# Kernel tuning notes

Measured on AMD Instinct MI355X. Metric: run time of the kernel, lower is better.

## Reference

```python
import jax, jax.numpy as jnp
import numpy as np

SINKHORN_ALPHA = 20.0
WEIGHT_LOSS_ECR = 100.0
OT_MAX_ITER = 100
STOP_THR = 0.005
EPS = 1e-16


def setup_inputs() -> dict:
    key = jax.random.key(0)
    # cost matrix: [num_topics, vocab]
    M = jax.random.uniform(key, (512, 65536), dtype=jnp.float32)
    return {"M": M}


def reference(M) -> jnp.ndarray:
    n, m = M.shape
    a = jnp.full((n, 1), 1.0 / n, dtype=M.dtype)   # row marginal
    b = jnp.full((m, 1), 1.0 / m, dtype=M.dtype)   # col marginal
    u0 = jnp.full((n, 1), 1.0 / n, dtype=M.dtype)
    K = jnp.exp(-M * SINKHORN_ALPHA)               # [n, m]

    def cond_fn(carry):
        u, v, err, cpt = carry
        return (err > STOP_THR) & (cpt < OT_MAX_ITER)

    def body_fn(carry):
        u, v, err, cpt = carry
        v = b / (K.T @ u + EPS)                    # [m, 1]
        u = a / (K @ v + EPS)                      # [n, 1]
        cpt = cpt + 1
        # convergence check every 50 iters (cpt % 50 == 1), matching torch loop
        err = jax.lax.cond(
            cpt % 50 == 1,
            lambda: jnp.sum(jnp.abs(v * (K.T @ u) - b)).astype(err.dtype),
            lambda: err,
        )
        return (u, v, err, cpt)

    init = (u0, jnp.zeros((m, 1), dtype=M.dtype), jnp.asarray(1.0, M.dtype), jnp.asarray(0, jnp.int32))
    u, v, _, _ = jax.lax.while_loop(cond_fn, body_fn, init)

    transp = u * (K * v.T)                         # [n, m] transport plan
    loss_ECR = jnp.sum(transp * M) * WEIGHT_LOSS_ECR
    return loss_ECR
```

## Files before the change

### kernel.cpp

```cpp
#include <hip/hip_runtime.h>

#define NROW 512
#define NCOL 65536
#define BANDS 4

static __device__ __forceinline__ float wave_sum(float x) {
  #pragma unroll
  for (int off = 32; off; off >>= 1) x += __shfl_down(x, off, 64);
  return x;
}

static __device__ __forceinline__ void gbar(int* cnt, int* phase) {
  __syncthreads();
  if (threadIdx.x == 0) {
    int ph = atomicAdd(phase, 0);
    __threadfence();
    if (atomicAdd(cnt, 1) == (int)gridDim.x - 1) {
      atomicExch(cnt, 0);
      __threadfence();
      atomicAdd(phase, 1);
    } else {
      while (atomicAdd(phase, 0) == ph) { __builtin_amdgcn_s_sleep(8); }
    }
    __threadfence();
  }
  __syncthreads();
}

static __device__ __forceinline__ unsigned short f2bf(float f) {
  unsigned int u = __float_as_uint(f);
  u += 0x7FFFu + ((u >> 16) & 1u);
  return (unsigned short)(u >> 16);
}
static __device__ __forceinline__ float bf2f_lo(unsigned int w) {
  return __uint_as_float(w << 16);
}
static __device__ __forceinline__ float bf2f_hi(unsigned int w) {
  return __uint_as_float(w & 0xFFFF0000u);
}

__global__ __launch_bounds__(512)
void k1a_colsum(const float* __restrict__ M, unsigned short* __restrict__ E16,
                float* __restrict__ tPart, float* __restrict__ eA,
                int* __restrict__ bar) {
  const int tid = threadIdx.x, bid = blockIdx.x;
  const int colblk = bid & 255, band = bid >> 8;
  const int chunk = tid & 63;
  const int part  = tid >> 6;
  const int col0  = (colblk << 8) + (chunk << 2);
  const int r0    = (band << 7) + (part << 4);

  __shared__ float sCol[8 * 256];

  if (bid == 0 && tid < 8) eA[tid] = 0.f;
  if (bid == 0 && tid < 2) bar[tid] = 0;

  const float* Mp = M + (size_t)r0 * NCOL + col0;
  unsigned short* Ep = E16 + (size_t)r0 * NCOL + col0;
  float4 cs = {0.f, 0.f, 0.f, 0.f};
  #pragma unroll 8
  for (int rr = 0; rr < 16; ++rr) {
    float4 m = *(const float4*)(Mp + (size_t)rr * NCOL);
    float e0 = __expf(-20.f * m.x), e1 = __expf(-20.f * m.y);
    float e2 = __expf(-20.f * m.z), e3 = __expf(-20.f * m.w);
    cs.x += e0; cs.y += e1; cs.z += e2; cs.w += e3;
    uint2 w;
    w.x = (unsigned int)f2bf(e0) | ((unsigned int)f2bf(e1) << 16);
    w.y = (unsigned int)f2bf(e2) | ((unsigned int)f2bf(e3) << 16);
    *(uint2*)(Ep + (size_t)rr * NCOL) = w;
  }
  *(float4*)(sCol + part * 256 + (chunk << 2)) = cs;
  __syncthreads();
  if (tid < 256) {
    float t = 0.f;
    #pragma unroll
    for (int p = 0; p < 8; ++p) t += sCol[p * 256 + tid];
    tPart[(size_t)band * NCOL + (colblk << 8) + tid] = t;
  }
}

__global__ __launch_bounds__(256)
void k1b_v1(const float* __restrict__ tPart, float* __restrict__ v) {
  const int gid = blockIdx.x * 256 + threadIdx.x;
  const int col0 = gid << 2;
  const float am = 1.0f / NROW, bm = 1.0f / NCOL, EPSV = 1e-16f;
  float4 t = {0.f, 0.f, 0.f, 0.f};
  #pragma unroll
  for (int b = 0; b < BANDS; ++b) {
    float4 p = *(const float4*)(tPart + (size_t)b * NCOL + col0);
    t.x += p.x; t.y += p.y; t.z += p.z; t.w += p.w;
  }
  float4 vv = {bm / (t.x * am + EPSV), bm / (t.y * am + EPSV),
               bm / (t.z * am + EPSV), bm / (t.w * am + EPSV)};
  *(float4*)(v + col0) = vv;
}

__global__ __launch_bounds__(1024)
void k2_rowdot(const unsigned short* __restrict__ E16,
               const float* __restrict__ v, float* __restrict__ u) {
  const int tid = threadIdx.x, row = blockIdx.x;
  const float am = 1.0f / NROW, EPSV = 1e-16f;
  const uint4* E4 = (const uint4*)(E16 + (size_t)row * NCOL);
  const float4* V4 = (const float4*)v;
  __shared__ float sRed[16];

  float acc = 0.f;
  #pragma unroll 4
  for (int it = 0; it < NCOL / 8 / 1024; ++it) {
    const int c = (it << 10) + tid;
    uint4 w = E4[c];
    float4 va = V4[2 * c], vb = V4[2 * c + 1];
    acc += bf2f_lo(w.x) * va.x + bf2f_hi(w.x) * va.y
         + bf2f_lo(w.y) * va.z + bf2f_hi(w.y) * va.w
         + bf2f_lo(w.z) * vb.x + bf2f_hi(w.z) * vb.y
         + bf2f_lo(w.w) * vb.z + bf2f_hi(w.w) * vb.w;
  }
  acc = wave_sum(acc);
  if ((tid & 63) == 0) sRed[tid >> 6] = acc;
  __syncthreads();
  if (tid == 0) {
    float s = 0.f;
    #pragma unroll
    for (int w = 0; w < 16; ++w) s += sRed[w];
    u[row] = am / (s + EPSV);
  }
}

__global__ __launch_bounds__(512)
void k3a_colsum_u(const unsigned short* __restrict__ E16,
                  const float* __restrict__ v, const float* __restrict__ u,
                  float* __restrict__ tPart, float* __restrict__ eA) {
  const int tid = threadIdx.x, bid = blockIdx.x;
  const int colblk = bid & 255, band = bid >> 8;
  const int chunk = tid & 63;
  const int part  = tid >> 6;
  const int col0  = (colblk << 8) + (chunk << 2);
  const int r0l   = part << 4;

  __shared__ float sU[128];
  __shared__ float sCol[8 * 256];
  __shared__ float sRed[8];

  if (tid < 128) sU[tid] = u[(band << 7) + tid];
  __syncthreads();

  const float4 vv = *(const float4*)(v + col0);
  const unsigned short* Ep = E16 + (size_t)((band << 7) + r0l) * NCOL + col0;
  float4 cs = {0.f, 0.f, 0.f, 0.f};
  float lacc = 0.f;
  #pragma unroll 8
  for (int rr = 0; rr < 16; ++rr) {
    uint2 w = *(const uint2*)(Ep + (size_t)rr * NCOL);
    float e0 = bf2f_lo(w.x), e1 = bf2f_hi(w.x);
    float e2 = bf2f_lo(w.y), e3 = bf2f_hi(w.y);
    float us = sU[r0l + rr];
    cs.x = fmaf(e0, us, cs.x);
    cs.y = fmaf(e1, us, cs.y);
    cs.z = fmaf(e2, us, cs.z);
    cs.w = fmaf(e3, us, cs.w);
    float m0 = __logf(e0) * (-0.05f);
    float m1 = __logf(e1) * (-0.05f);
    float m2 = __logf(e2) * (-0.05f);
    float m3 = __logf(e3) * (-0.05f);
    lacc += us * (e0 * m0 * vv.x + e1 * m1 * vv.y
                + e2 * m2 * vv.z + e3 * m3 * vv.w);
  }
  *(float4*)(sCol + part * 256 + (chunk << 2)) = cs;
  lacc = wave_sum(lacc);
  if ((tid & 63) == 0) sRed[tid >> 6] = lacc;
  __syncthreads();
  if (tid < 256) {
    float t = 0.f;
    #pragma unroll
    for (int p = 0; p < 8; ++p) t += sCol[p * 256 + tid];
    tPart[(size_t)band * NCOL + (colblk << 8) + tid] = t;
  }
  if (tid == 0)
    atomicAdd(&eA[2], sRed[0] + sRed[1] + sRed[2] + sRed[3]
                    + sRed[4] + sRed[5] + sRed[6] + sRed[7]);
}

__global__ __launch_bounds__(256)
void k3b_err(const float* __restrict__ tPart, const float* __restrict__ v,
             float* __restrict__ tArr, float* __restrict__ eA,
             float* __restrict__ out, int* __restrict__ done) {
  const int tid = threadIdx.x;
  const int gid = blockIdx.x * 256 + tid;
  const int col0 = gid << 2;
  const float bm = 1.0f / NCOL;
  __shared__ float sRed[4];

  float4 t = {0.f, 0.f, 0.f, 0.f};
  #pragma unroll
  for (int b = 0; b < BANDS; ++b) {
    float4 p = *(const float4*)(tPart + (size_t)b * NCOL + col0);
    t.x += p.x; t.y += p.y; t.z += p.z; t.w += p.w;
  }
  *(float4*)(tArr + col0) = t;
  float4 vv = *(const float4*)(v + col0);
  float pe = fabsf(vv.x * t.x - bm) + fabsf(vv.y * t.y - bm)
           + fabsf(vv.z * t.z - bm) + fabsf(vv.w * t.w - bm);
  pe = wave_sum(pe);
  if ((tid & 63) == 0) sRed[tid >> 6] = pe;
  __syncthreads();
  if (tid == 0) {
    atomicAdd(&eA[0], sRed[0] + sRed[1] + sRed[2] + sRed[3]);
    __threadfence();
    int old = atomicAdd((int*)(eA + 4), 1);
    if (old == (int)gridDim.x - 1) {
      __threadfence();
      float err = atomicAdd(&eA[0], 0.f);
      float ls  = atomicAdd(&eA[2], 0.f);
      if (err <= 0.005f) { out[0] = 100.f * ls; done[0] = 1; }
      else               { out[0] = 0.f;        done[0] = 0; }
    }
  }
}

__global__ __launch_bounds__(1024)
void k5_fallback(const float* __restrict__ M, float* __restrict__ out,
                 float* __restrict__ v, float* __restrict__ u,
                 const float* __restrict__ tArr, float* __restrict__ eA,
                 const int* __restrict__ done, int* __restrict__ bar) {
  if (done[0]) return;
  const int tid = threadIdx.x, bid = blockIdx.x;
  const float am = 1.0f / NROW, bm = 1.0f / NCOL, EPSV = 1e-16f;
  int* cnt = bar;
  int* phs = bar + 1;

  __shared__ float sU[NROW];
  __shared__ float sCol[16 * 256];
  __shared__ float sRedA[16], sRedB[16];
  __shared__ float sErr;

  const int chunk = tid & 63;
  const int part  = tid >> 6;
  const int col0  = (bid << 8) + (chunk << 2);
  const int r0    = part << 5;
  const int row0  = bid << 1;

  float tt = (tid < 256) ? tArr[(bid << 8) + tid] : 0.f;

  int cpt = 1;
  while (true) {
    if (tid < 256) v[(bid << 8) + tid] = bm / (tt + EPSV);
    gbar(cnt, phs);
    cpt++;

    {
      const float4* M40 = (const float4*)M + (size_t)row0 * (NCOL / 4);
      const float4* M41 = (const float4*)M + (size_t)(row0 + 1) * (NCOL / 4);
      const float4* V4  = (const float4*)v;
      float ra = 0.f, rb = 0.f;
      #pragma unroll 4
      for (int it = 0; it < NCOL / 4 / 1024; ++it) {
        const int c = (it << 10) + tid;
        float4 vv = V4[c];
        float4 m0 = M40[c], m1 = M41[c];
        ra += __expf(-20.f * m0.x) * vv.x + __expf(-20.f * m0.y) * vv.y
            + __expf(-20.f * m0.z) * vv.z + __expf(-20.f * m0.w) * vv.w;
        rb += __expf(-20.f * m1.x) * vv.x + __expf(-20.f * m1.y) * vv.y
            + __expf(-20.f * m1.z) * vv.z + __expf(-20.f * m1.w) * vv.w;
      }
      ra = wave_sum(ra); rb = wave_sum(rb);
      if ((tid & 63) == 0) { sRedA[tid >> 6] = ra; sRedB[tid >> 6] = rb; }
      __syncthreads();
      if (tid < 2) {
        const float* sr = (tid == 0) ? sRedA : sRedB;
        float s = 0.f;
        #pragma unroll
        for (int w = 0; w < 16; ++w) s += sr[w];
        u[row0 + tid] = am / (s + EPSV);
      }
    }
    gbar(cnt, phs);
    if (cpt >= 100) break;

    if (tid < NROW) sU[tid] = u[tid];
    __syncthreads();
    float4 cs = {0.f, 0.f, 0.f, 0.f};
    #pragma unroll 4
    for (int r = r0; r < r0 + 32; ++r) {
      float4 m = *(const float4*)(M + (size_t)r * NCOL + col0);
      float us = sU[r];
      cs.x = fmaf(__expf(-20.f * m.x), us, cs.x);
      cs.y = fmaf(__expf(-20.f * m.y), us, cs.y);
      cs.z = fmaf(__expf(-20.f * m.z), us, cs.z);
      cs.w = fmaf(__expf(-20.f * m.w), us, cs.w);
    }
    *(float4*)(sCol + part * 256 + (chunk << 2)) = cs;
    __syncthreads();
    if (tid < 256) {
      tt = 0.f;
      #pragma unroll
      for (int p = 0; p < 16; ++p) tt += sCol[p * 256 + tid];
    }

    if (cpt == 51) {
      float pe = (tid < 256) ? fabsf(v[(bid << 8) + tid] * tt - bm) : 0.f;
      pe = wave_sum(pe);
      __syncthreads();
      if ((tid & 63) == 0) sRedA[tid >> 6] = pe;
      __syncthreads();
      if (tid == 0) {
        float s = 0.f;
        #pragma unroll
        for (int w = 0; w < 16; ++w) s += sRedA[w];
        atomicAdd(&eA[1], s);
      }
      gbar(cnt, phs);
      if (tid == 0) sErr = atomicAdd(&eA[1], 0.f);
      __syncthreads();
      if (sErr <= 0.005f) break;
    }
  }

  __syncthreads();
  if (tid < NROW) sU[tid] = u[tid];
  __syncthreads();
  {
    const float4 vv = *(const float4*)(v + col0);
    float lacc = 0.f;
    #pragma unroll 4
    for (int r = r0; r < r0 + 32; ++r) {
      float4 m = *(const float4*)(M + (size_t)r * NCOL + col0);
      float us = sU[r];
      lacc += us * (__expf(-20.f * m.x) * m.x * vv.x
                  + __expf(-20.f * m.y) * m.y * vv.y
                  + __expf(-20.f * m.z) * m.z * vv.z
                  + __expf(-20.f * m.w) * m.w * vv.w);
    }
    lacc = wave_sum(lacc);
    if ((tid & 63) == 0) sRedA[tid >> 6] = lacc;
    __syncthreads();
    if (tid == 0) {
      float s = 0.f;
      #pragma unroll
      for (int w = 0; w < 16; ++w) s += sRedA[w];
      atomicAdd(out, 100.f * s);
    }
  }
}

extern "C" void kernel_launch(void* const* d_in, const int* in_sizes, int n_in,
                              void* d_out, int out_size, void* d_ws, size_t ws_size,
                              hipStream_t stream) {
  const float* M = (const float*)d_in[0];
  float* out = (float*)d_out;

  const size_t offV = 0;
  const size_t offT = offV + (size_t)NCOL * sizeof(float);
  const size_t offU = offT + (size_t)NCOL * sizeof(float);
  const size_t offE = offU + 4096;
  const size_t offD = offE + 256;
  const size_t offB = offD + 256;
  const size_t offP = offB + 256;
  const size_t offE16 = offP + (size_t)BANDS * NCOL * sizeof(float);
  const size_t need = offE16 + (size_t)NROW * NCOL * sizeof(unsigned short);
  if (ws_size < need) return;

  char* ws = (char*)d_ws;
  float* v     = (float*)(ws + offV);
  float* tArr  = (float*)(ws + offT);
  float* u     = (float*)(ws + offU);
  float* eA    = (float*)(ws + offE);
  int*   done  = (int*)(ws + offD);
  int*   bar   = (int*)(ws + offB);
  float* tPart = (float*)(ws + offP);
  unsigned short* E16 = (unsigned short*)(ws + offE16);

  k1a_colsum  <<<dim3(1024), dim3(512),  0, stream>>>(M, E16, tPart, eA, bar);
  k1b_v1      <<<dim3(64),   dim3(256),  0, stream>>>(tPart, v);
  k2_rowdot   <<<dim3(512),  dim3(1024), 0, stream>>>(E16, v, u);
  k3a_colsum_u<<<dim3(1024), dim3(512),  0, stream>>>(E16, v, u, tPart, eA);
  k3b_err     <<<dim3(64),   dim3(256),  0, stream>>>(tPart, v, tArr, eA, out, done);
  k5_fallback <<<dim3(256),  dim3(1024), 0, stream>>>(M, out, v, u, tArr, eA,
                                                      done, bar);
}
```

Before: 243.0 us.

## Remap column-sum blocks to full row span and fuse finalize kernels

Column-sum kernels now assign each block all 512 rows over a 64-column slice, so column totals complete inside a block. This lets v and the error/loss reduction be computed in the same kernel, removing the two small follow-up kernels and the banded partial-sum buffer. In exchange, each row access is narrower (256-byte segments), which may reduce memory coalescing efficiency, and the blocks carry a larger shared reduction.

```diff
diff --git a/kernel.cpp b/kernel.cpp
--- a/kernel.cpp
+++ b/kernel.cpp
@@ -2,7 +2,6 @@
 
 #define NROW 512
 #define NCOL 65536
-#define BANDS 4
 
 static __device__ __forceinline__ float wave_sum(float x) {
   #pragma unroll
@@ -40,17 +39,17 @@
 }
 
 __global__ __launch_bounds__(512)
-void k1a_colsum(const float* __restrict__ M, unsigned short* __restrict__ E16,
-                float* __restrict__ tPart, float* __restrict__ eA,
-                int* __restrict__ bar) {
+void k1_colsum(const float* __restrict__ M, unsigned short* __restrict__ E16,
+               float* __restrict__ v, float* __restrict__ eA,
+               int* __restrict__ bar) {
   const int tid = threadIdx.x, bid = blockIdx.x;
-  const int colblk = bid & 255, band = bid >> 8;
-  const int chunk = tid & 63;
-  const int part  = tid >> 6;
-  const int col0  = (colblk << 8) + (chunk << 2);
-  const int r0    = (band << 7) + (part << 4);
-
-  __shared__ float sCol[8 * 256];
+  const int chunk = tid & 15;
+  const int part  = tid >> 4;
+  const int col0  = (bid << 6) + (chunk << 2);
+  const int r0    = part << 4;
+  const float am = 1.0f / NROW, bm = 1.0f / NCOL, EPSV = 1e-16f;
+
+  __shared__ float sCol[32 * 64];
 
   if (bid == 0 && tid < 8) eA[tid] = 0.f;
   if (bid == 0 && tid < 2) bar[tid] = 0;
@@ -69,30 +68,14 @@
     w.y = (unsigned int)f2bf(e2) | ((unsigned int)f2bf(e3) << 16);
     *(uint2*)(Ep + (size_t)rr * NCOL) = w;
   }
-  *(float4*)(sCol + part * 256 + (chunk << 2)) = cs;
-  __syncthreads();
-  if (tid < 256) {
+  *(float4*)(sCol + part * 64 + (chunk << 2)) = cs;
+  __syncthreads();
+  if (tid < 64) {
     float t = 0.f;
     #pragma unroll
-    for (int p = 0; p < 8; ++p) t += sCol[p * 256 + tid];
-    tPart[(size_t)band * NCOL + (colblk << 8) + tid] = t;
-  }
-}
-
-__global__ __launch_bounds__(256)
-void k1b_v1(const float* __restrict__ tPart, float* __restrict__ v) {
-  const int gid = blockIdx.x * 256 + threadIdx.x;
-  const int col0 = gid << 2;
-  const float am = 1.0f / NROW, bm = 1.0f / NCOL, EPSV = 1e-16f;
-  float4 t = {0.f, 0.f, 0.f, 0.f};
-  #pragma unroll
-  for (int b = 0; b < BANDS; ++b) {
-    float4 p = *(const float4*)(tPart + (size_t)b * NCOL + col0);
-    t.x += p.x; t.y += p.y; t.z += p.z; t.w += p.w;
-  }
-  float4 vv = {bm / (t.x * am + EPSV), bm / (t.y * am + EPSV),
-               bm / (t.z * am + EPSV), bm / (t.w * am + EPSV)};
-  *(float4*)(v + col0) = vv;
+    for (int p = 0; p < 32; ++p) t += sCol[p * 64 + tid];
+    v[(bid << 6) + tid] = bm / (t * am + EPSV);
+  }
 }
 
 __global__ __launch_bounds__(1024)
@@ -127,25 +110,26 @@
 }
 
 __global__ __launch_bounds__(512)
-void k3a_colsum_u(const unsigned short* __restrict__ E16,
-                  const float* __restrict__ v, const float* __restrict__ u,
-                  float* __restrict__ tPart, float* __restrict__ eA) {
+void k3_colsum_u(const unsigned short* __restrict__ E16,
+                 const float* __restrict__ v, const float* __restrict__ u,
+                 float* __restrict__ tArr, float* __restrict__ eA,
+                 float* __restrict__ out, int* __restrict__ done) {
   const int tid = threadIdx.x, bid = blockIdx.x;
-  const int colblk = bid & 255, band = bid >> 8;
-  const int chunk = tid & 63;
-  const int part  = tid >> 6;
-  const int col0  = (colblk << 8) + (chunk << 2);
-  const int r0l   = part << 4;
-
-  __shared__ float sU[128];
-  __shared__ float sCol[8 * 256];
+  const int chunk = tid & 15;
+  const int part  = tid >> 4;
+  const int col0  = (bid << 6) + (chunk << 2);
+  const int r0    = part << 4;
+  const float bm = 1.0f / NCOL;
+
+  __shared__ float sU[NROW];
+  __shared__ float sCol[32 * 64];
   __shared__ float sRed[8];
 
-  if (tid < 128) sU[tid] = u[(band << 7) + tid];
+  sU[tid] = u[tid];
   __syncthreads();
 
   const float4 vv = *(const float4*)(v + col0);
-  const unsigned short* Ep = E16 + (size_t)((band << 7) + r0l) * NCOL + col0;
+  const unsigned short* Ep = E16 + (size_t)r0 * NCOL + col0;
   float4 cs = {0.f, 0.f, 0.f, 0.f};
   float lacc = 0.f;
   #pragma unroll 8
@@ -153,7 +137,7 @@
     uint2 w = *(const uint2*)(Ep + (size_t)rr * NCOL);
     float e0 = bf2f_lo(w.x), e1 = bf2f_hi(w.x);
     float e2 = bf2f_lo(w.y), e3 = bf2f_hi(w.y);
-    float us = sU[r0l + rr];
+    float us = sU[r0 + rr];
     cs.x = fmaf(e0, us, cs.x);
     cs.y = fmaf(e1, us, cs.y);
     cs.z = fmaf(e2, us, cs.z);
@@ -165,46 +149,28 @@
     lacc += us * (e0 * m0 * vv.x + e1 * m1 * vv.y
                 + e2 * m2 * vv.z + e3 * m3 * vv.w);
   }
-  *(float4*)(sCol + part * 256 + (chunk << 2)) = cs;
+  *(float4*)(sCol + part * 64 + (chunk << 2)) = cs;
   lacc = wave_sum(lacc);
   if ((tid & 63) == 0) sRed[tid >> 6] = lacc;
   __syncthreads();
-  if (tid < 256) {
+
+  float lblk = 0.f;
+  if (tid == 0) {
+    #pragma unroll
+    for (int w = 0; w < 8; ++w) lblk += sRed[w];
+  }
+  float pe = 0.f;
+  if (tid < 64) {
     float t = 0.f;
     #pragma unroll
-    for (int p = 0; p < 8; ++p) t += sCol[p * 256 + tid];
-    tPart[(size_t)band * NCOL + (colblk << 8) + tid] = t;
-  }
-  if (tid == 0)
-    atomicAdd(&eA[2], sRed[0] + sRed[1] + sRed[2] + sRed[3]
-                    + sRed[4] + sRed[5] + sRed[6] + sRed[7]);
-}
-
-__global__ __launch_bounds__(256)
-void k3b_err(const float* __restrict__ tPart, const float* __restrict__ v,
-             float* __restrict__ tArr, float* __restrict__ eA,
-             float* __restrict__ out, int* __restrict__ done) {
-  const int tid = threadIdx.x;
-  const int gid = blockIdx.x * 256 + tid;
-  const int col0 = gid << 2;
-  const float bm = 1.0f / NCOL;
-  __shared__ float sRed[4];
-
-  float4 t = {0.f, 0.f, 0.f, 0.f};
-  #pragma unroll
-  for (int b = 0; b < BANDS; ++b) {
-    float4 p = *(const float4*)(tPart + (size_t)b * NCOL + col0);
-    t.x += p.x; t.y += p.y; t.z += p.z; t.w += p.w;
-  }
-  *(float4*)(tArr + col0) = t;
-  float4 vv = *(const float4*)(v + col0);
-  float pe = fabsf(vv.x * t.x - bm) + fabsf(vv.y * t.y - bm)
-           + fabsf(vv.z * t.z - bm) + fabsf(vv.w * t.w - bm);
+    for (int p = 0; p < 32; ++p) t += sCol[p * 64 + tid];
+    tArr[(bid << 6) + tid] = t;
+    pe = fabsf(v[(bid << 6) + tid] * t - bm);
+  }
   pe = wave_sum(pe);
-  if ((tid & 63) == 0) sRed[tid >> 6] = pe;
-  __syncthreads();
   if (tid == 0) {
-    atomicAdd(&eA[0], sRed[0] + sRed[1] + sRed[2] + sRed[3]);
+    atomicAdd(&eA[0], pe);
+    atomicAdd(&eA[2], lblk);
     __threadfence();
     int old = atomicAdd((int*)(eA + 4), 1);
     if (old == (int)gridDim.x - 1) {
@@ -354,26 +320,23 @@
   const size_t offE = offU + 4096;
   const size_t offD = offE + 256;
   const size_t offB = offD + 256;
-  const size_t offP = offB + 256;
-  const size_t offE16 = offP + (size_t)BANDS * NCOL * sizeof(float);
+  const size_t offE16 = offB + 256;
   const size_t need = offE16 + (size_t)NROW * NCOL * sizeof(unsigned short);
   if (ws_size < need) return;
 
   char* ws = (char*)d_ws;
-  float* v     = (float*)(ws + offV);
-  float* tArr  = (float*)(ws + offT);
-  float* u     = (float*)(ws + offU);
-  float* eA    = (float*)(ws + offE);
-  int*   done  = (int*)(ws + offD);
-  int*   bar   = (int*)(ws + offB);
-  float* tPart = (float*)(ws + offP);
+  float* v    = (float*)(ws + offV);
+  float* tArr = (float*)(ws + offT);
+  float* u    = (float*)(ws + offU);
+  float* eA   = (float*)(ws + offE);
+  int*   done = (int*)(ws + offD);
+  int*   bar  = (int*)(ws + offB);
   unsigned short* E16 = (unsigned short*)(ws + offE16);
 
-  k1a_colsum  <<<dim3(1024), dim3(512),  0, stream>>>(M, E16, tPart, eA, bar);
-  k1b_v1      <<<dim3(64),   dim3(256),  0, stream>>>(tPart, v);
-  k2_rowdot   <<<dim3(512),  dim3(1024), 0, stream>>>(E16, v, u);
-  k3a_colsum_u<<<dim3(1024), dim3(512),  0, stream>>>(E16, v, u, tPart, eA);
-  k3b_err     <<<dim3(64),   dim3(256),  0, stream>>>(tPart, v, tArr, eA, out, done);
-  k5_fallback <<<dim3(256),  dim3(1024), 0, stream>>>(M, out, v, u, tArr, eA,
-                                                      done, bar);
-}
+  k1_colsum  <<<dim3(1024), dim3(512),  0, stream>>>(M, E16, v, eA, bar);
+  k2_rowdot  <<<dim3(512),  dim3(1024), 0, stream>>>(E16, v, u);
+  k3_colsum_u<<<dim3(1024), dim3(512),  0, stream>>>(E16, v, u, tArr, eA,
+                                                     out, done);
+  k5_fallback<<<dim3(256),  dim3(1024), 0, stream>>>(M, out, v, u, tArr, eA,
+                                                     done, bar);
+}
```

Measured after the change: 269.1 us. 1.11x slower.
